# Performance work log

Hardware: AMD Instinct MI355X
Metric: run time of the kernel (lower is better)

## Reference

```python
import jax, jax.numpy as jnp
import numpy as np

D_MODEL = 256
NHEAD = 8
NUM_EXPERTS = 5
LQ, LK, BATCH = 100, 1024, 16
LN_EPS = 1e-5


def setup_inputs() -> dict:
    key = jax.random.key(0)
    ks = jax.random.split(key, 12)
    d, E = D_MODEL, NUM_EXPERTS
    s = 1.0 / np.sqrt(d)
    return {
        "tgt": jax.random.normal(ks[0], (LQ, BATCH, d), jnp.float32),
        "memory": jax.random.normal(ks[1], (LK, BATCH, d), jnp.float32),
        "query_pos": jax.random.normal(ks[2], (LQ, BATCH, d), jnp.float32),
        "pos": jax.random.normal(ks[3], (LK, BATCH, d), jnp.float32),
        # per-expert MultiheadAttention params (packed q,k,v in_proj like torch)
        "w_in": jax.random.normal(ks[4], (E, 3 * d, d), jnp.float32) * s,
        "b_in": jnp.zeros((E, 3 * d), jnp.float32),
        "w_out": jax.random.normal(ks[5], (E, d, d), jnp.float32) * s,
        "b_out": jnp.zeros((E, d), jnp.float32),
        # gating network
        "w_gate": jax.random.normal(ks[6], (E, d), jnp.float32) * s,
        "b_gate": jnp.zeros((E,), jnp.float32),
        # LayerNorm
        "ln_gamma": jnp.ones((d,), jnp.float32),
        "ln_beta": jnp.zeros((d,), jnp.float32),
    }


def _moe_cross_attn(tgt, memory, query_pos, pos, w_in, b_in, w_out, b_out,
                    w_gate, b_gate, ln_gamma, ln_beta):
    Lq, B, d = tgt.shape
    H = NHEAD
    hd = d // H
    E = w_in.shape[0]
    Lk = memory.shape[0]

    # gating over (seq*batch, d) -> softmax over experts
    gate = jax.nn.softmax(tgt @ w_gate.T + b_gate, axis=-1)  # (Lq, B, E)

    q_emb = tgt + query_pos      # (Lq, B, d)
    k_emb = memory + pos         # (Lk, B, d)

    wq, wk, wv = w_in[:, :d], w_in[:, d:2 * d], w_in[:, 2 * d:]
    bq, bk, bv = b_in[:, :d], b_in[:, d:2 * d], b_in[:, 2 * d:]

    # batched projections across all experts (replaces python loop of MHA calls)
    q = jnp.einsum('lbd,eod->elbo', q_emb, wq) + bq[:, None, None, :]
    k = jnp.einsum('sbd,eod->esbo', k_emb, wk) + bk[:, None, None, :]
    v = jnp.einsum('sbd,eod->esbo', memory, wv) + bv[:, None, None, :]

    q = q.reshape(E, Lq, B, H, hd) * (1.0 / np.sqrt(hd))
    k = k.reshape(E, Lk, B, H, hd)
    v = v.reshape(E, Lk, B, H, hd)

    scores = jnp.einsum('elbhk,esbhk->ebhls', q, k)      # (E, B, H, Lq, Lk)
    attn = jax.nn.softmax(scores, axis=-1)
    ctx = jnp.einsum('ebhls,esbhk->elbhk', attn, v).reshape(E, Lq, B, d)

    out = jnp.einsum('elbd,eod->elbo', ctx, w_out) + b_out[:, None, None, :]

    # softmax-gated weighted combine of expert outputs
    mo = jnp.einsum('lbe,elbd->lbd', gate, out)

    x = tgt + mo  # dropout is identity (p=0.0)
    mu = jnp.mean(x, axis=-1, keepdims=True)
    var = jnp.var(x, axis=-1, keepdims=True)
    return (x - mu) * jax.lax.rsqrt(var + LN_EPS) * ln_gamma + ln_beta


def reference(tgt, memory, query_pos, pos, w_in, b_in, w_out, b_out,
              w_gate, b_gate, ln_gamma, ln_beta):
    return _moe_cross_attn(tgt, memory, query_pos, pos, w_in, b_in, w_out,
                           b_out, w_gate, b_gate, ln_gamma, ln_beta)
```

## Files before the change

### kernel.cpp

```cpp
#include <hip/hip_runtime.h>


typedef __bf16 bf16x8 __attribute__((ext_vector_type(8)));
typedef float f32x4 __attribute__((ext_vector_type(4)));
typedef unsigned int u32x4 __attribute__((ext_vector_type(4)));
typedef unsigned int u32x2 __attribute__((ext_vector_type(2)));
typedef unsigned short u16x4 __attribute__((ext_vector_type(4)));
typedef unsigned short us;

__device__ __forceinline__ us f2bf(float f) {
    unsigned u = __builtin_bit_cast(unsigned, f);
    u += 0x7FFFu + ((u >> 16) & 1u);
    return (us)(u >> 16);
}

__device__ __forceinline__ unsigned pack2(float lo, float hi) {
    return (unsigned)f2bf(lo) | ((unsigned)f2bf(hi) << 16);
}

__device__ __forceinline__ float bf2f(us v) {
    unsigned u = ((unsigned)v) << 16;
    return __builtin_bit_cast(float, u);
}

__device__ __forceinline__ bf16x8 ld_bf8(const us* p) {
    return __builtin_bit_cast(bf16x8, *reinterpret_cast<const u32x4*>(p));
}

__device__ __forceinline__ void gld_lds16(const us* g, us* l) {
    __builtin_amdgcn_global_load_lds(
        (const __attribute__((address_space(1))) unsigned int*)g,
        (__attribute__((address_space(3))) unsigned int*)l, 16, 0, 0);
}

__launch_bounds__(256)
__global__ void cvt_all(const float* __restrict__ tgt, const float* __restrict__ qpos,
                        const float* __restrict__ mem, const float* __restrict__ pos,
                        const float* __restrict__ w_in, const float* __restrict__ w_out,
                        const float* __restrict__ w_gate, const float* __restrict__ b_gate,
                        us* __restrict__ Aq, us* __restrict__ Ak, us* __restrict__ Av,
                        us* __restrict__ Wb, us* __restrict__ WOb,
                        float* __restrict__ Gate)
{
    const int bid = blockIdx.x;
    const int tid = threadIdx.x;
    if (bid < 400) {
        const int i = bid * 256 + tid;
        const int lane = tid & 63;
        const int row = i >> 6;
        f32x4 a = reinterpret_cast<const f32x4*>(tgt)[i];
        f32x4 b = reinterpret_cast<const f32x4*>(qpos)[i];
        u16x4 r;
#pragma unroll
        for (int j = 0; j < 4; ++j) r[j] = f2bf(a[j] + b[j]);
        reinterpret_cast<u16x4*>(Aq)[i] = r;
        float g[5];
#pragma unroll
        for (int e = 0; e < 5; ++e) {
            f32x4 wg = *reinterpret_cast<const f32x4*>(w_gate + e * 256 + 4 * lane);
            float p = a[0] * wg[0] + a[1] * wg[1] + a[2] * wg[2] + a[3] * wg[3];
#pragma unroll
            for (int off = 32; off >= 1; off >>= 1) p += __shfl_xor(p, off, 64);
            g[e] = p + b_gate[e];
        }
        float mx = g[0];
#pragma unroll
        for (int e = 1; e < 5; ++e) mx = fmaxf(mx, g[e]);
        float sm = 0.0f;
#pragma unroll
        for (int e = 0; e < 5; ++e) { g[e] = __expf(g[e] - mx); sm += g[e]; }
        const float invs = 1.0f / sm;
        if (lane == 0) {
#pragma unroll
            for (int e = 0; e < 5; ++e) Gate[row * 5 + e] = g[e] * invs;
        }
    } else if (bid < 4496) {
        int i = (bid - 400) * 256 + tid;
        f32x4 m = reinterpret_cast<const f32x4*>(mem)[i];
        f32x4 p = reinterpret_cast<const f32x4*>(pos)[i];
        u16x4 rk, rv;
#pragma unroll
        for (int j = 0; j < 4; ++j) { rk[j] = f2bf(m[j] + p[j]); rv[j] = f2bf(m[j]); }
        reinterpret_cast<u16x4*>(Ak)[i] = rk;
        reinterpret_cast<u16x4*>(Av)[i] = rv;
    } else if (bid < 5456) {
        int i = (bid - 4496) * 256 + tid;
        f32x4 a = reinterpret_cast<const f32x4*>(w_in)[i];
        u16x4 r;
#pragma unroll
        for (int j = 0; j < 4; ++j) r[j] = f2bf(a[j]);
        const int e    = i / 49152;
        const int rem  = i % 49152;
        const int row  = rem >> 6;
        const int kq4  = rem & 63;
        const int role = row >> 8;
        const int col  = row & 255;
        const int g    = kq4 >> 1;
        const int sub  = kq4 & 1;
        const size_t dst = (size_t)(e * 3 + role) * 65536
                         + ((size_t)(g * 256 + col)) * 8 + sub * 4;
        *reinterpret_cast<u16x4*>(Wb + dst) = r;
    } else {
        int i = (bid - 5456) * 256 + tid;
        f32x4 a = reinterpret_cast<const f32x4*>(w_out)[i];
        u16x4 r;
#pragma unroll
        for (int j = 0; j < 4; ++j) r[j] = f2bf(a[j]);
        reinterpret_cast<u16x4*>(WOb)[i] = r;
    }
}

__launch_bounds__(256, 4)
__global__ void gemm_qkv(const us* __restrict__ Aq, const us* __restrict__ Ak,
                         const us* __restrict__ Av, const us* __restrict__ Wb,
                         const float* __restrict__ b_in,
                         us* __restrict__ Qb, us* __restrict__ Kb, us* __restrict__ Vb)
{
    const int rb   = blockIdx.x;
    const int col0 = blockIdx.y * 128;
    const int zr   = blockIdx.z;
    const us* A; const us* W; const float* bias; us* C;
    float scale; int M;
    if (zr < 5) {
        if (rb >= 13) return;
        A = Aq; W = Wb + (size_t)zr * 196608; bias = b_in + (size_t)zr * 768;
        C = Qb + (size_t)zr * 409600; scale = 0.17677669529663687f; M = 1600;
    } else if (zr < 10) {
        const int e = zr - 5;
        A = Ak; W = Wb + 65536 + (size_t)e * 196608; bias = b_in + (size_t)e * 768 + 256;
        C = Kb + (size_t)e * 4194304; scale = 1.0f; M = 16384;
    } else {
        const int e = zr - 10;
        A = Av; W = Wb + 131072 + (size_t)e * 196608; bias = b_in + (size_t)e * 768 + 512;
        C = Vb + (size_t)e * 4194304; scale = 1.0f; M = 16384;
    }
    const int row0 = rb * 128;

    __shared__ us As[2 * 8192];
    const int tid  = threadIdx.x;
    const int lane = tid & 63;
    const int w    = tid >> 6;
    const int l15  = lane & 15;
    const int quad = lane >> 4;
    const int wm   = (w >> 1) * 64;
    const int wn   = (w & 1) * 64;
    const int srow = lane >> 3;
    const int gofs = ((lane & 7) ^ srow) * 8;

    auto stageA = [&](int buf, int kt) {
#pragma unroll
        for (int cc = 0; cc < 4; ++cc) {
            const int c = w * 4 + cc;
            gld_lds16(A + (size_t)(row0 + c * 8 + srow) * 256 + kt * 64 + gofs,
                      &As[buf * 8192 + c * 512]);
        }
    };

    f32x4 acc[4][4] = {};

    stageA(0, 0);
    __builtin_amdgcn_sched_barrier(0);

#pragma unroll
    for (int kt = 0; kt < 4; ++kt) {
        const int cur = kt & 1;
        u32x4 bf[2][4];
#pragma unroll
        for (int kh = 0; kh < 2; ++kh)
#pragma unroll
            for (int ni = 0; ni < 4; ++ni)
                bf[kh][ni] = *reinterpret_cast<const u32x4*>(
                    W + (((size_t)(kt * 8 + kh * 4 + quad) * 256
                          + (col0 + wn + ni * 16 + l15)) * 8));
        __builtin_amdgcn_sched_barrier(0);
        if (kt < 3) stageA(cur ^ 1, kt + 1);
        __builtin_amdgcn_sched_barrier(0);
        if (kt < 3) asm volatile("s_waitcnt vmcnt(4)" ::: "memory");
        else        asm volatile("s_waitcnt vmcnt(0)" ::: "memory");
        __builtin_amdgcn_s_barrier();
        __builtin_amdgcn_sched_barrier(0);
#pragma unroll
        for (int kh = 0; kh < 2; ++kh) {
            bf16x8 af[4];
#pragma unroll
            for (int mi = 0; mi < 4; ++mi) {
                const int row = wm + mi * 16 + l15;
                const int seg = (kh * 4 + quad) ^ (row & 7);
                af[mi] = ld_bf8(&As[cur * 8192 + row * 64 + seg * 8]);
            }
#pragma unroll
            for (int mi = 0; mi < 4; ++mi)
#pragma unroll
                for (int ni = 0; ni < 4; ++ni)
                    acc[mi][ni] = __builtin_amdgcn_mfma_f32_16x16x32_bf16(
                        __builtin_bit_cast(bf16x8, bf[kh][ni]), af[mi], acc[mi][ni], 0, 0, 0);
        }
        if (kt < 3) {
            asm volatile("s_waitcnt lgkmcnt(0)" ::: "memory");
            __builtin_amdgcn_sched_barrier(0);
            __builtin_amdgcn_s_barrier();
            __builtin_amdgcn_sched_barrier(0);
        }
    }

#pragma unroll
    for (int mi = 0; mi < 4; ++mi) {
        const int row = row0 + wm + mi * 16 + l15;
        if (row < M) {
#pragma unroll
            for (int ni = 0; ni < 4; ++ni) {
                const int colb = col0 + wn + ni * 16 + quad * 4;
                const f32x4 b4 = *reinterpret_cast<const f32x4*>(bias + colb);
                u32x2 pk;
                pk[0] = pack2((acc[mi][ni][0] + b4[0]) * scale,
                              (acc[mi][ni][1] + b4[1]) * scale);
                pk[1] = pack2((acc[mi][ni][2] + b4[2]) * scale,
                              (acc[mi][ni][3] + b4[3]) * scale);
                *reinterpret_cast<u32x2*>(C + (size_t)row * 256 + colb) = pk;
            }
        }
    }
}

__launch_bounds__(256)
__global__ void gemm_og(const us* __restrict__ PO, const float* __restrict__ PL,
                        const us* __restrict__ WOb, const float* __restrict__ b_out,
                        float* __restrict__ OUTf)
{
    if (blockIdx.x >= 13) return;
    const int e = blockIdx.z;
    const us* W = WOb + (size_t)e * 65536;
    const float* bias = b_out + (size_t)e * 256;
    float* Cout = OUTf + (size_t)e * 409600;

    const int row0 = blockIdx.x * 128;
    const int col0 = blockIdx.y * 128;
    __shared__ us As[2 * 8192];
    __shared__ us Bs[2 * 8192];
    const int tid  = threadIdx.x;
    const int lane = tid & 63;
    const int w    = tid >> 6;
    const int l15  = lane & 15;
    const int quad = lane >> 4;
    const int wm   = (w >> 1) * 64;
    const int wn   = (w & 1) * 64;
    const int srow = lane >> 3;
    const int gofs = ((lane & 7) ^ srow) * 8;

    u32x4 POr[4][2];
    float Lr[4];

    auto loadA = [&](int kt) {
#pragma unroll
        for (int cc = 0; cc < 4; ++cc) {
            const int c = w * 4 + cc;
            int grow = row0 + c * 8 + srow;
            if (grow > 1599) grow = 1599;
            const int d0 = kt * 64 + gofs;
            const size_t base = (size_t)e * 409600 + (size_t)grow * 256 + d0;
#pragma unroll
            for (int s = 0; s < 2; ++s)
                POr[cc][s] = *reinterpret_cast<const u32x4*>(PO + base + (size_t)s * 2048000);
            const int l = grow >> 4, bb = grow & 15, hh = d0 >> 5;
            float L = 0.0f;
#pragma unroll
            for (int s = 0; s < 2; ++s)
                L += PL[((((size_t)s * 5 + e) * 16 + bb) * 8 + hh) * 128 + l];
            Lr[cc] = L;
        }
    };
    auto writeA = [&](int buf) {
#pragma unroll
        for (int cc = 0; cc < 4; ++cc) {
            const float inv = 1.0f / Lr[cc];
            u32x4 pk;
#pragma unroll
            for (int j = 0; j < 4; ++j) {
                float v0 = 0.0f, v1 = 0.0f;
#pragma unroll
                for (int s = 0; s < 2; ++s) {
                    const unsigned u = POr[cc][s][j];
                    v0 += __builtin_bit_cast(float, u << 16);
                    v1 += __builtin_bit_cast(float, u & 0xffff0000u);
                }
                pk[j] = pack2(v0 * inv, v1 * inv);
            }
            *reinterpret_cast<u32x4*>(&As[buf * 8192 + (w * 4 + cc) * 512 + lane * 8]) = pk;
        }
    };
    auto loadW = [&](int buf, int kt) {
#pragma unroll
        for (int cc = 0; cc < 4; ++cc) {
            const int c = w * 4 + cc;
            const int row = c * 8 + srow;
            gld_lds16(W + (size_t)(col0 + row) * 256 + kt * 64 + gofs,
                      &Bs[buf * 8192 + c * 512]);
        }
    };

    loadA(0);
    loadW(0, 0);
    writeA(0);
    __syncthreads();

    f32x4 acc[4][4] = {};

#pragma unroll
    for (int kt = 0; kt < 4; ++kt) {
        const int cur = kt & 1;
        if (kt < 3) {
            loadA(kt + 1);
            loadW(cur ^ 1, kt + 1);
        }
#pragma unroll
        for (int kh = 0; kh < 2; ++kh) {
            bf16x8 af[4], bf[4];
#pragma unroll
            for (int mi = 0; mi < 4; ++mi) {
                const int row = wm + mi * 16 + l15;
                const int seg = (kh * 4 + quad) ^ (row & 7);
                af[mi] = ld_bf8(&As[cur * 8192 + row * 64 + seg * 8]);
            }
#pragma unroll
            for (int ni = 0; ni < 4; ++ni) {
                const int col = wn + ni * 16 + l15;
                const int seg = (kh * 4 + quad) ^ (col & 7);
                bf[ni] = ld_bf8(&Bs[cur * 8192 + col * 64 + seg * 8]);
            }
#pragma unroll
            for (int mi = 0; mi < 4; ++mi)
#pragma unroll
                for (int ni = 0; ni < 4; ++ni)
                    acc[mi][ni] = __builtin_amdgcn_mfma_f32_16x16x32_bf16(bf[ni], af[mi], acc[mi][ni], 0, 0, 0);
        }
        if (kt < 3) {
            writeA(cur ^ 1);
            __syncthreads();
        }
    }

#pragma unroll
    for (int mi = 0; mi < 4; ++mi) {
        const int row = row0 + wm + mi * 16 + l15;
        if (row < 1600) {
#pragma unroll
            for (int ni = 0; ni < 4; ++ni) {
                const int colb = col0 + wn + ni * 16 + quad * 4;
                const f32x4 b4 = *reinterpret_cast<const f32x4*>(bias + colb);
                f32x4 v;
#pragma unroll
                for (int r = 0; r < 4; ++r) v[r] = acc[mi][ni][r] + b4[r];
                *reinterpret_cast<f32x4*>(Cout + (size_t)row * 256 + colb) = v;
            }
        }
    }
}

__device__ __forceinline__ int vrow(int d) { return d * 264 + 8 * (d >> 3); }

__launch_bounds__(512)
__global__ void attn(const us* __restrict__ Qb, const us* __restrict__ Kb,
                     const us* __restrict__ Vb, us* __restrict__ PO,
                     float* __restrict__ PL)
{
    const int z = blockIdx.x;
    const int h = blockIdx.y;
    const int sp = blockIdx.z;
    const int e = z >> 4, b = z & 15;
    const int tid  = threadIdx.x;
    const int w    = tid >> 6;
    const int lane = tid & 63;
    const int l15  = lane & 15, quad = lane >> 4;
    __shared__ us Ks[256 * 32];
    __shared__ us Vs[8464];
    __shared__ us Ps[7][2][16 * 40];

    u32x4 qraw = {0u, 0u, 0u, 0u};
    if (w < 7) {
        const int l = w * 16 + l15;
        if (l < 100)
            qraw = *reinterpret_cast<const u32x4*>(
                Qb + ((size_t)((e * 100 + l) * 16 + b)) * 256 + h * 32 + quad * 8);
    }
    const bf16x8 qf = __builtin_bit_cast(bf16x8, qraw);

    const f32x4 zacc = {};
    f32x4 o0 = {}, o1 = {};
    float lsum = 0.0f;

    for (int sc = 0; sc < 2; ++sc) {
        const int key0 = (sp * 2 + sc) * 256;
        if (sc) __syncthreads();
        {
            const int kl  = lane >> 2;
            const int seg = lane & 3;
            const us* kg = Kb + ((size_t)((e * 1024 + key0 + w * 16 + kl) * 16 + b)) * 256
                              + h * 32 + seg * 8;
            gld_lds16(kg, &Ks[w * 512]);
            gld_lds16(kg + (size_t)128 * 16 * 256, &Ks[4096 + w * 512]);

            const int kv = tid >> 2;
            const int sg = tid & 3;
            const us* vg = Vb + ((size_t)((e * 1024 + key0 + kv) * 16 + b)) * 256
                              + h * 32 + sg * 8;
            u32x4 v0 = *reinterpret_cast<const u32x4*>(vg);
            u32x4 v1 = *reinterpret_cast<const u32x4*>(vg + (size_t)128 * 16 * 256);
#pragma unroll
            for (int j = 0; j < 4; ++j) {
                const int d0 = sg * 8 + 2 * j;
                const int e0 = vrow(d0);
                const int e1 = e0 + 264;
                Vs[e0 + kv]       = (us)(v0[j] & 0xffff);
                Vs[e1 + kv]       = (us)(v0[j] >> 16);
                Vs[e0 + 128 + kv] = (us)(v1[j] & 0xffff);
                Vs[e1 + 128 + kv] = (us)(v1[j] >> 16);
            }
        }
        __syncthreads();

        if (w < 7) {
            auto qk = [&](int c) {
                bf16x8 kf0 = ld_bf8(&Ks[(c * 32 + l15) * 32 + quad * 8]);
                bf16x8 kf1 = ld_bf8(&Ks[(c * 32 + 16 + l15) * 32 + quad * 8]);
                f32x4 s0 = __builtin_amdgcn_mfma_f32_16x16x32_bf16(kf0, qf, zacc, 0, 0, 0);
                f32x4 s1 = __builtin_amdgcn_mfma_f32_16x16x32_bf16(kf1, qf, zacc, 0, 0, 0);
                float p0[4], p1[4];
#pragma unroll
                for (int r = 0; r < 4; ++r) {
                    p0[r] = __expf(s0[r]);
                    p1[r] = __expf(s1[r]);
                    lsum += p0[r] + p1[r];
                }
                u32x2 w0, w1;
                w0[0] = pack2(p0[0], p0[1]);
                w0[1] = pack2(p0[2], p0[3]);
                w1[0] = pack2(p1[0], p1[1]);
                w1[1] = pack2(p1[2], p1[3]);
                us* psb = &Ps[w][c & 1][0];
                *reinterpret_cast<u32x2*>(&psb[l15 * 40 + quad * 4])      = w0;
                *reinterpret_cast<u32x2*>(&psb[l15 * 40 + 16 + quad * 4]) = w1;
            };
            auto pv = [&](int c) {
                bf16x8 pf  = ld_bf8(&Ps[w][c & 1][l15 * 40 + quad * 8]);
                bf16x8 vf0 = ld_bf8(&Vs[vrow(l15) + c * 32 + quad * 8]);
                bf16x8 vf1 = ld_bf8(&Vs[vrow(16 + l15) + c * 32 + quad * 8]);
                o0 = __builtin_amdgcn_mfma_f32_16x16x32_bf16(pf, vf0, o0, 0, 0, 0);
                o1 = __builtin_amdgcn_mfma_f32_16x16x32_bf16(pf, vf1, o1, 0, 0, 0);
            };
            qk(0);
#pragma unroll
            for (int c = 1; c < 8; ++c) {
                qk(c);
                pv(c - 1);
            }
            pv(7);
        }
    }

    if (w >= 7) return;

    lsum += __shfl_xor(lsum, 16, 64);
    lsum += __shfl_xor(lsum, 32, 64);

#pragma unroll
    for (int r = 0; r < 4; ++r) {
        const int row = w * 16 + quad * 4 + r;
        if (row < 100) {
            const size_t o = (((size_t)((sp * 5 + e) * 100 + row)) * 16 + b) * 256 + h * 32;
            PO[o + l15]      = f2bf(o0[r]);
            PO[o + 16 + l15] = f2bf(o1[r]);
        }
    }
    const int q = w * 16 + l15;
    if (quad == 0 && q < 100)
        PL[((((size_t)sp * 5 + e) * 16 + b) * 8 + h) * 128 + q] = lsum;
}

__launch_bounds__(256)
__global__ void finalize(const float* __restrict__ tgt, const float* __restrict__ Gate,
                         const float* __restrict__ OUTf,
                         const float* __restrict__ gamma, const float* __restrict__ beta,
                         float* __restrict__ out)
{
    const int row = blockIdx.x;
    const int d = threadIdx.x;
    __shared__ float red[8];
    const float t = tgt[(size_t)row * 256 + d];

    float mo = 0.0f;
#pragma unroll
    for (int e = 0; e < 5; ++e)
        mo += Gate[row * 5 + e] * OUTf[((size_t)e * 1600 + row) * 256 + d];
    const float x = t + mo;

    float p1 = x, p2 = x * x;
#pragma unroll
    for (int off = 32; off >= 1; off >>= 1) {
        p1 += __shfl_xor(p1, off, 64);
        p2 += __shfl_xor(p2, off, 64);
    }
    if ((d & 63) == 0) { red[d >> 6] = p1; red[4 + (d >> 6)] = p2; }
    __syncthreads();
    const float mean = (red[0] + red[1] + red[2] + red[3]) * (1.0f / 256.0f);
    const float msq  = (red[4] + red[5] + red[6] + red[7]) * (1.0f / 256.0f);
    const float var  = msq - mean * mean;

    out[(size_t)row * 256 + d] = (x - mean) * rsqrtf(var + 1e-5f) * gamma[d] + beta[d];
}

extern "C" void kernel_launch(void* const* d_in, const int* in_sizes, int n_in,
                              void* d_out, int out_size, void* d_ws, size_t ws_size,
                              hipStream_t stream)
{
    const float* tgt    = (const float*)d_in[0];
    const float* mem    = (const float*)d_in[1];
    const float* qpos   = (const float*)d_in[2];
    const float* pos    = (const float*)d_in[3];
    const float* w_in   = (const float*)d_in[4];
    const float* b_in   = (const float*)d_in[5];
    const float* w_out  = (const float*)d_in[6];
    const float* b_out  = (const float*)d_in[7];
    const float* w_gate = (const float*)d_in[8];
    const float* b_gate = (const float*)d_in[9];
    const float* ln_g   = (const float*)d_in[10];
    const float* ln_b   = (const float*)d_in[11];
    float* out = (float*)d_out;

    char* p = (char*)d_ws;
    auto alloc = [&](size_t n) { char* r = p; p += (n + 255) & ~(size_t)255; return r; };

    us* Aq   = (us*)alloc(409600ull * 2);
    us* Ak   = (us*)alloc(4194304ull * 2);
    us* Av   = (us*)alloc(4194304ull * 2);
    us* Wb   = (us*)alloc(983040ull * 2);
    us* WOb  = (us*)alloc(327680ull * 2);
    us* Qb   = (us*)alloc(5ull * 409600 * 2);
    us* Kb   = (us*)alloc(5ull * 4194304 * 2);
    us* Vb   = (us*)alloc(5ull * 4194304 * 2);
    float* OUTf  = (float*)alloc(5ull * 409600 * 4);
    float* Gate  = (float*)alloc(1600ull * 5 * 4);
    us*    PO = (us*)d_ws;
    float* PL = (float*)((char*)d_ws + 8192000);

    cvt_all<<<5776, 256, 0, stream>>>(tgt, qpos, mem, pos, w_in, w_out,
                                      w_gate, b_gate, Aq, Ak, Av, Wb, WOb, Gate);

    gemm_qkv<<<dim3(128, 2, 15), 256, 0, stream>>>(Aq, Ak, Av, Wb, b_in, Qb, Kb, Vb);

    attn<<<dim3(80, 8, 2), 512, 0, stream>>>(Qb, Kb, Vb, PO, PL);

    gemm_og<<<dim3(16, 2, 5), 256, 0, stream>>>(PO, PL, WOb, b_out, OUTf);

    finalize<<<1600, 256, 0, stream>>>(tgt, Gate, OUTf, ln_g, ln_b, out);
}
```

Before: 192.4 us.

## Store K/V projections in head-major layout for contiguous attention loads

The projection GEMM epilogue for K and V experts (zr>=5) now writes output in an [e][h][b][key][32] layout instead of row-major [key][b][256]. The attention kernel reads K and V tiles from this layout, so each (e,b,h) block streams contiguous 64-byte rows instead of strided 64-byte pieces spaced 8KB apart. This is meant to improve DRAM/cache locality of the attention loads, at the cost of scattered 8-byte stores in the GEMM epilogue. The new addressing assumes M is an exact multiple of the tile, since the row<M bounds check was dropped for that branch.

```diff
diff --git a/kernel.cpp b/kernel.cpp
--- a/kernel.cpp
+++ b/kernel.cpp
@@ -203,10 +203,30 @@
         }
     }
 
-#pragma unroll
-    for (int mi = 0; mi < 4; ++mi) {
-        const int row = row0 + wm + mi * 16 + l15;
-        if (row < M) {
+    if (zr < 5) {
+#pragma unroll
+        for (int mi = 0; mi < 4; ++mi) {
+            const int row = row0 + wm + mi * 16 + l15;
+            if (row < M) {
+#pragma unroll
+                for (int ni = 0; ni < 4; ++ni) {
+                    const int colb = col0 + wn + ni * 16 + quad * 4;
+                    const f32x4 b4 = *reinterpret_cast<const f32x4*>(bias + colb);
+                    u32x2 pk;
+                    pk[0] = pack2((acc[mi][ni][0] + b4[0]) * scale,
+                                  (acc[mi][ni][1] + b4[1]) * scale);
+                    pk[1] = pack2((acc[mi][ni][2] + b4[2]) * scale,
+                                  (acc[mi][ni][3] + b4[3]) * scale);
+                    *reinterpret_cast<u32x2*>(C + (size_t)row * 256 + colb) = pk;
+                }
+            }
+        }
+    } else {
+#pragma unroll
+        for (int mi = 0; mi < 4; ++mi) {
+            const int row = row0 + wm + mi * 16 + l15;
+            const int key = row >> 4;
+            const int b   = row & 15;
 #pragma unroll
             for (int ni = 0; ni < 4; ++ni) {
                 const int colb = col0 + wn + ni * 16 + quad * 4;
@@ -216,7 +236,9 @@
                               (acc[mi][ni][1] + b4[1]) * scale);
                 pk[1] = pack2((acc[mi][ni][2] + b4[2]) * scale,
                               (acc[mi][ni][3] + b4[3]) * scale);
-                *reinterpret_cast<u32x2*>(C + (size_t)row * 256 + colb) = pk;
+                const size_t dst = ((((size_t)(colb >> 5) * 16 + b) * 1024) + key) * 32
+                                 + (colb & 31);
+                *reinterpret_cast<u32x2*>(C + dst) = pk;
             }
         }
     }
@@ -375,6 +397,8 @@
     __shared__ us Vs[8464];
     __shared__ us Ps[7][2][16 * 40];
 
+    const size_t hvbase = (((size_t)(e * 8 + h) * 16 + b) * 1024) * 32;
+
     u32x4 qraw = {0u, 0u, 0u, 0u};
     if (w < 7) {
         const int l = w * 16 + l15;
@@ -394,17 +418,15 @@
         {
             const int kl  = lane >> 2;
             const int seg = lane & 3;
-            const us* kg = Kb + ((size_t)((e * 1024 + key0 + w * 16 + kl) * 16 + b)) * 256
-                              + h * 32 + seg * 8;
+            const us* kg = Kb + hvbase + (size_t)(key0 + w * 16 + kl) * 32 + seg * 8;
             gld_lds16(kg, &Ks[w * 512]);
-            gld_lds16(kg + (size_t)128 * 16 * 256, &Ks[4096 + w * 512]);
+            gld_lds16(kg + (size_t)128 * 32, &Ks[4096 + w * 512]);
 
             const int kv = tid >> 2;
             const int sg = tid & 3;
-            const us* vg = Vb + ((size_t)((e * 1024 + key0 + kv) * 16 + b)) * 256
-                              + h * 32 + sg * 8;
+            const us* vg = Vb + hvbase + (size_t)(key0 + kv) * 32 + sg * 8;
             u32x4 v0 = *reinterpret_cast<const u32x4*>(vg);
-            u32x4 v1 = *reinterpret_cast<const u32x4*>(vg + (size_t)128 * 16 * 256);
+            u32x4 v1 = *reinterpret_cast<const u32x4*>(vg + (size_t)128 * 32);
 #pragma unroll
             for (int j = 0; j < 4; ++j) {
                 const int d0 = sg * 8 + 2 * j;
```

Result: no change. 194.8 us (+1.2%).

## Widen QKV GEMM tiles to full 256 columns and drop attention key split

Applied to the files above, without the earlier changes.

The QKV projection now uses 512-thread blocks that each compute all 256 output columns for a 128-row tile. This halves the A-tile reloads and the grid size. The attention kernel no longer splits the 1024 keys across two blocks. Each block loops over all four 256-key chunks, which removes the partial-sum write and the reduction in the output-projection GEMM. In exchange, attention parallelism falls to 640 blocks and the GEMM blocks carry higher register and LDS pressure, which could hurt occupancy.

```diff
diff --git a/kernel.cpp b/kernel.cpp
--- a/kernel.cpp
+++ b/kernel.cpp
@@ -110,15 +110,14 @@
     }
 }
 
-__launch_bounds__(256, 4)
+__launch_bounds__(512, 4)
 __global__ void gemm_qkv(const us* __restrict__ Aq, const us* __restrict__ Ak,
                          const us* __restrict__ Av, const us* __restrict__ Wb,
                          const float* __restrict__ b_in,
                          us* __restrict__ Qb, us* __restrict__ Kb, us* __restrict__ Vb)
 {
-    const int rb   = blockIdx.x;
-    const int col0 = blockIdx.y * 128;
-    const int zr   = blockIdx.z;
+    const int rb = blockIdx.x;
+    const int zr = blockIdx.y;
     const us* A; const us* W; const float* bias; us* C;
     float scale; int M;
     if (zr < 5) {
@@ -142,15 +141,15 @@
     const int w    = tid >> 6;
     const int l15  = lane & 15;
     const int quad = lane >> 4;
-    const int wm   = (w >> 1) * 64;
-    const int wn   = (w & 1) * 64;
+    const int wm   = (w >> 2) * 64;
+    const int wn   = (w & 3) * 64;
     const int srow = lane >> 3;
     const int gofs = ((lane & 7) ^ srow) * 8;
 
     auto stageA = [&](int buf, int kt) {
 #pragma unroll
-        for (int cc = 0; cc < 4; ++cc) {
-            const int c = w * 4 + cc;
+        for (int cc = 0; cc < 2; ++cc) {
+            const int c = w * 2 + cc;
             gld_lds16(A + (size_t)(row0 + c * 8 + srow) * 256 + kt * 64 + gofs,
                       &As[buf * 8192 + c * 512]);
         }
@@ -171,11 +170,11 @@
             for (int ni = 0; ni < 4; ++ni)
                 bf[kh][ni] = *reinterpret_cast<const u32x4*>(
                     W + (((size_t)(kt * 8 + kh * 4 + quad) * 256
-                          + (col0 + wn + ni * 16 + l15)) * 8));
+                          + (wn + ni * 16 + l15)) * 8));
         __builtin_amdgcn_sched_barrier(0);
         if (kt < 3) stageA(cur ^ 1, kt + 1);
         __builtin_amdgcn_sched_barrier(0);
-        if (kt < 3) asm volatile("s_waitcnt vmcnt(4)" ::: "memory");
+        if (kt < 3) asm volatile("s_waitcnt vmcnt(2)" ::: "memory");
         else        asm volatile("s_waitcnt vmcnt(0)" ::: "memory");
         __builtin_amdgcn_s_barrier();
         __builtin_amdgcn_sched_barrier(0);
@@ -209,7 +208,7 @@
         if (row < M) {
 #pragma unroll
             for (int ni = 0; ni < 4; ++ni) {
-                const int colb = col0 + wn + ni * 16 + quad * 4;
+                const int colb = wn + ni * 16 + quad * 4;
                 const f32x4 b4 = *reinterpret_cast<const f32x4*>(bias + colb);
                 u32x2 pk;
                 pk[0] = pack2((acc[mi][ni][0] + b4[0]) * scale,
@@ -247,7 +246,7 @@
     const int srow = lane >> 3;
     const int gofs = ((lane & 7) ^ srow) * 8;
 
-    u32x4 POr[4][2];
+    u32x4 POr[4];
     float Lr[4];
 
     auto loadA = [&](int kt) {
@@ -257,16 +256,10 @@
             int grow = row0 + c * 8 + srow;
             if (grow > 1599) grow = 1599;
             const int d0 = kt * 64 + gofs;
-            const size_t base = (size_t)e * 409600 + (size_t)grow * 256 + d0;
-#pragma unroll
-            for (int s = 0; s < 2; ++s)
-                POr[cc][s] = *reinterpret_cast<const u32x4*>(PO + base + (size_t)s * 2048000);
+            POr[cc] = *reinterpret_cast<const u32x4*>(
+                PO + (size_t)e * 409600 + (size_t)grow * 256 + d0);
             const int l = grow >> 4, bb = grow & 15, hh = d0 >> 5;
-            float L = 0.0f;
-#pragma unroll
-            for (int s = 0; s < 2; ++s)
-                L += PL[((((size_t)s * 5 + e) * 16 + bb) * 8 + hh) * 128 + l];
-            Lr[cc] = L;
+            Lr[cc] = PL[(((size_t)e * 16 + bb) * 8 + hh) * 128 + l];
         }
     };
     auto writeA = [&](int buf) {
@@ -276,13 +269,9 @@
             u32x4 pk;
 #pragma unroll
             for (int j = 0; j < 4; ++j) {
-                float v0 = 0.0f, v1 = 0.0f;
-#pragma unroll
-                for (int s = 0; s < 2; ++s) {
-                    const unsigned u = POr[cc][s][j];
-                    v0 += __builtin_bit_cast(float, u << 16);
-                    v1 += __builtin_bit_cast(float, u & 0xffff0000u);
-                }
+                const unsigned u = POr[cc][j];
+                const float v0 = __builtin_bit_cast(float, u << 16);
+                const float v1 = __builtin_bit_cast(float, u & 0xffff0000u);
                 pk[j] = pack2(v0 * inv, v1 * inv);
             }
             *reinterpret_cast<u32x4*>(&As[buf * 8192 + (w * 4 + cc) * 512 + lane * 8]) = pk;
@@ -365,7 +354,6 @@
 {
     const int z = blockIdx.x;
     const int h = blockIdx.y;
-    const int sp = blockIdx.z;
     const int e = z >> 4, b = z & 15;
     const int tid  = threadIdx.x;
     const int w    = tid >> 6;
@@ -388,8 +376,8 @@
     f32x4 o0 = {}, o1 = {};
     float lsum = 0.0f;
 
-    for (int sc = 0; sc < 2; ++sc) {
-        const int key0 = (sp * 2 + sc) * 256;
+    for (int sc = 0; sc < 4; ++sc) {
+        const int key0 = sc * 256;
         if (sc) __syncthreads();
         {
             const int kl  = lane >> 2;
@@ -466,14 +454,14 @@
     for (int r = 0; r < 4; ++r) {
         const int row = w * 16 + quad * 4 + r;
         if (row < 100) {
-            const size_t o = (((size_t)((sp * 5 + e) * 100 + row)) * 16 + b) * 256 + h * 32;
+            const size_t o = (((size_t)(e * 100 + row)) * 16 + b) * 256 + h * 32;
             PO[o + l15]      = f2bf(o0[r]);
             PO[o + 16 + l15] = f2bf(o1[r]);
         }
     }
     const int q = w * 16 + l15;
     if (quad == 0 && q < 100)
-        PL[((((size_t)sp * 5 + e) * 16 + b) * 8 + h) * 128 + q] = lsum;
+        PL[(((size_t)e * 16 + b) * 8 + h) * 128 + q] = lsum;
 }
 
 __launch_bounds__(256)
@@ -540,14 +528,14 @@
     float* OUTf  = (float*)alloc(5ull * 409600 * 4);
     float* Gate  = (float*)alloc(1600ull * 5 * 4);
     us*    PO = (us*)d_ws;
-    float* PL = (float*)((char*)d_ws + 8192000);
+    float* PL = (float*)((char*)d_ws + 4096000);
 
     cvt_all<<<5776, 256, 0, stream>>>(tgt, qpos, mem, pos, w_in, w_out,
                                       w_gate, b_gate, Aq, Ak, Av, Wb, WOb, Gate);
 
-    gemm_qkv<<<dim3(128, 2, 15), 256, 0, stream>>>(Aq, Ak, Av, Wb, b_in, Qb, Kb, Vb);
-
-    attn<<<dim3(80, 8, 2), 512, 0, stream>>>(Qb, Kb, Vb, PO, PL);
+    gemm_qkv<<<dim3(128, 15), 512, 0, stream>>>(Aq, Ak, Av, Wb, b_in, Qb, Kb, Vb);
+
+    attn<<<dim3(80, 8), 512, 0, stream>>>(Qb, Kb, Vb, PO, PL);
 
     gemm_og<<<dim3(16, 2, 5), 256, 0, stream>>>(PO, PL, WOb, b_out, OUTf);
 
```

Result: slower. 199.1 us (+3.5%).

## Fuse K/V projection into attention kernel, drop materialized K/V buffers

Applied to the files above, without the earlier changes.

Removes the K and V projection GEMM and their large bf16 intermediate buffers. Each attention block now computes its own 256-key by 32-dim K and V head slices with MFMA directly from the converted memory/pos activations and the packed weights, then writes them into shared memory. This avoids writing and re-reading roughly 80 MB of K/V through HBM. The cost is redundant work: the same key rows are re-read for every head, and the projection loads go straight from global memory with no LDS staging. Only the Q projection remains a separate GEMM, and the PO/PL workspace now gets its own allocations.

```diff
diff --git a/kernel.cpp b/kernel.cpp
--- a/kernel.cpp
+++ b/kernel.cpp
@@ -111,29 +111,18 @@
 }
 
 __launch_bounds__(256, 4)
-__global__ void gemm_qkv(const us* __restrict__ Aq, const us* __restrict__ Ak,
-                         const us* __restrict__ Av, const us* __restrict__ Wb,
-                         const float* __restrict__ b_in,
-                         us* __restrict__ Qb, us* __restrict__ Kb, us* __restrict__ Vb)
+__global__ void gemm_q(const us* __restrict__ Aq, const us* __restrict__ Wb,
+                       const float* __restrict__ b_in, us* __restrict__ Qb)
 {
     const int rb   = blockIdx.x;
     const int col0 = blockIdx.y * 128;
-    const int zr   = blockIdx.z;
-    const us* A; const us* W; const float* bias; us* C;
-    float scale; int M;
-    if (zr < 5) {
-        if (rb >= 13) return;
-        A = Aq; W = Wb + (size_t)zr * 196608; bias = b_in + (size_t)zr * 768;
-        C = Qb + (size_t)zr * 409600; scale = 0.17677669529663687f; M = 1600;
-    } else if (zr < 10) {
-        const int e = zr - 5;
-        A = Ak; W = Wb + 65536 + (size_t)e * 196608; bias = b_in + (size_t)e * 768 + 256;
-        C = Kb + (size_t)e * 4194304; scale = 1.0f; M = 16384;
-    } else {
-        const int e = zr - 10;
-        A = Av; W = Wb + 131072 + (size_t)e * 196608; bias = b_in + (size_t)e * 768 + 512;
-        C = Vb + (size_t)e * 4194304; scale = 1.0f; M = 16384;
-    }
+    const int e    = blockIdx.z;
+    const us* A = Aq;
+    const us* W = Wb + (size_t)e * 196608;
+    const float* bias = b_in + (size_t)e * 768;
+    us* C = Qb + (size_t)e * 409600;
+    const float scale = 0.17677669529663687f;
+    const int M = 1600;
     const int row0 = rb * 128;
 
     __shared__ us As[2 * 8192];
@@ -359,9 +348,10 @@
 __device__ __forceinline__ int vrow(int d) { return d * 264 + 8 * (d >> 3); }
 
 __launch_bounds__(512)
-__global__ void attn(const us* __restrict__ Qb, const us* __restrict__ Kb,
-                     const us* __restrict__ Vb, us* __restrict__ PO,
-                     float* __restrict__ PL)
+__global__ void attn(const us* __restrict__ Qb, const us* __restrict__ Ak,
+                     const us* __restrict__ Av, const us* __restrict__ Wb,
+                     const float* __restrict__ b_in,
+                     us* __restrict__ PO, float* __restrict__ PL)
 {
     const int z = blockIdx.x;
     const int h = blockIdx.y;
@@ -375,6 +365,11 @@
     __shared__ us Vs[8464];
     __shared__ us Ps[7][2][16 * 40];
 
+    const us* Wk = Wb + (size_t)(e * 3 + 1) * 65536;
+    const us* Wv = Wb + (size_t)(e * 3 + 2) * 65536;
+    const float* bk_base = b_in + e * 768 + 256 + h * 32;
+    const float* bv_base = b_in + e * 768 + 512 + h * 32;
+
     u32x4 qraw = {0u, 0u, 0u, 0u};
     if (w < 7) {
         const int l = w * 16 + l15;
@@ -388,73 +383,106 @@
     f32x4 o0 = {}, o1 = {};
     float lsum = 0.0f;
 
+    auto compute = [&]() {
+        auto qk = [&](int c) {
+            bf16x8 kf0 = ld_bf8(&Ks[(c * 32 + l15) * 32 + quad * 8]);
+            bf16x8 kf1 = ld_bf8(&Ks[(c * 32 + 16 + l15) * 32 + quad * 8]);
+            f32x4 s0 = __builtin_amdgcn_mfma_f32_16x16x32_bf16(kf0, qf, zacc, 0, 0, 0);
+            f32x4 s1 = __builtin_amdgcn_mfma_f32_16x16x32_bf16(kf1, qf, zacc, 0, 0, 0);
+            float p0[4], p1[4];
+#pragma unroll
+            for (int r = 0; r < 4; ++r) {
+                p0[r] = __expf(s0[r]);
+                p1[r] = __expf(s1[r]);
+                lsum += p0[r] + p1[r];
+            }
+            u32x2 w0, w1;
+            w0[0] = pack2(p0[0], p0[1]);
+            w0[1] = pack2(p0[2], p0[3]);
+            w1[0] = pack2(p1[0], p1[1]);
+            w1[1] = pack2(p1[2], p1[3]);
+            us* psb = &Ps[w][c & 1][0];
+            *reinterpret_cast<u32x2*>(&psb[l15 * 40 + quad * 4])      = w0;
+            *reinterpret_cast<u32x2*>(&psb[l15 * 40 + 16 + quad * 4]) = w1;
+        };
+        auto pv = [&](int c) {
+            bf16x8 pf  = ld_bf8(&Ps[w][c & 1][l15 * 40 + quad * 8]);
+            bf16x8 vf0 = ld_bf8(&Vs[vrow(l15) + c * 32 + quad * 8]);
+            bf16x8 vf1 = ld_bf8(&Vs[vrow(16 + l15) + c * 32 + quad * 8]);
+            o0 = __builtin_amdgcn_mfma_f32_16x16x32_bf16(pf, vf0, o0, 0, 0, 0);
+            o1 = __builtin_amdgcn_mfma_f32_16x16x32_bf16(pf, vf1, o1, 0, 0, 0);
+        };
+        qk(0);
+#pragma unroll
+        for (int c = 1; c < 8; ++c) {
+            qk(c);
+            pv(c - 1);
+        }
+        pv(7);
+    };
+
     for (int sc = 0; sc < 2; ++sc) {
         const int key0 = (sp * 2 + sc) * 256;
         if (sc) __syncthreads();
+
         {
-            const int kl  = lane >> 2;
-            const int seg = lane & 3;
-            const us* kg = Kb + ((size_t)((e * 1024 + key0 + w * 16 + kl) * 16 + b)) * 256
-                              + h * 32 + seg * 8;
-            gld_lds16(kg, &Ks[w * 512]);
-            gld_lds16(kg + (size_t)128 * 16 * 256, &Ks[4096 + w * 512]);
-
-            const int kv = tid >> 2;
-            const int sg = tid & 3;
-            const us* vg = Vb + ((size_t)((e * 1024 + key0 + kv) * 16 + b)) * 256
-                              + h * 32 + sg * 8;
-            u32x4 v0 = *reinterpret_cast<const u32x4*>(vg);
-            u32x4 v1 = *reinterpret_cast<const u32x4*>(vg + (size_t)128 * 16 * 256);
-#pragma unroll
-            for (int j = 0; j < 4; ++j) {
-                const int d0 = sg * 8 + 2 * j;
-                const int e0 = vrow(d0);
-                const int e1 = e0 + 264;
-                Vs[e0 + kv]       = (us)(v0[j] & 0xffff);
-                Vs[e1 + kv]       = (us)(v0[j] >> 16);
-                Vs[e0 + 128 + kv] = (us)(v1[j] & 0xffff);
-                Vs[e1 + 128 + kv] = (us)(v1[j] >> 16);
+            const int wkey = w * 32;
+            f32x4 ka[2][2] = {};
+            f32x4 va[2][2] = {};
+#pragma unroll
+            for (int kt = 0; kt < 4; ++kt)
+#pragma unroll
+                for (int kh = 0; kh < 2; ++kh) {
+                    const int g = kt * 8 + kh * 4 + quad;
+                    u32x4 afk[2], afv[2], bk[2], bv[2];
+#pragma unroll
+                    for (int mi = 0; mi < 2; ++mi) {
+                        const size_t arow =
+                            (size_t)((key0 + wkey + mi * 16 + l15) * 16 + b) * 256
+                            + kt * 64 + kh * 32 + quad * 8;
+                        afk[mi] = *reinterpret_cast<const u32x4*>(Ak + arow);
+                        afv[mi] = *reinterpret_cast<const u32x4*>(Av + arow);
+                    }
+#pragma unroll
+                    for (int ni = 0; ni < 2; ++ni) {
+                        const size_t wof =
+                            ((size_t)g * 256 + (h * 32 + ni * 16 + l15)) * 8;
+                        bk[ni] = *reinterpret_cast<const u32x4*>(Wk + wof);
+                        bv[ni] = *reinterpret_cast<const u32x4*>(Wv + wof);
+                    }
+#pragma unroll
+                    for (int mi = 0; mi < 2; ++mi)
+#pragma unroll
+                        for (int ni = 0; ni < 2; ++ni) {
+                            ka[mi][ni] = __builtin_amdgcn_mfma_f32_16x16x32_bf16(
+                                __builtin_bit_cast(bf16x8, bk[ni]),
+                                __builtin_bit_cast(bf16x8, afk[mi]), ka[mi][ni], 0, 0, 0);
+                            va[mi][ni] = __builtin_amdgcn_mfma_f32_16x16x32_bf16(
+                                __builtin_bit_cast(bf16x8, bv[ni]),
+                                __builtin_bit_cast(bf16x8, afv[mi]), va[mi][ni], 0, 0, 0);
+                        }
+                }
+#pragma unroll
+            for (int mi = 0; mi < 2; ++mi) {
+                const int key = wkey + mi * 16 + l15;
+#pragma unroll
+                for (int ni = 0; ni < 2; ++ni) {
+                    const int d = ni * 16 + quad * 4;
+                    const f32x4 bk4 = *reinterpret_cast<const f32x4*>(bk_base + d);
+                    const f32x4 bv4 = *reinterpret_cast<const f32x4*>(bv_base + d);
+                    u32x2 pk;
+                    pk[0] = pack2(ka[mi][ni][0] + bk4[0], ka[mi][ni][1] + bk4[1]);
+                    pk[1] = pack2(ka[mi][ni][2] + bk4[2], ka[mi][ni][3] + bk4[3]);
+                    *reinterpret_cast<u32x2*>(&Ks[key * 32 + d]) = pk;
+#pragma unroll
+                    for (int r = 0; r < 4; ++r)
+                        Vs[vrow(d + r) + key] = f2bf(va[mi][ni][r] + bv4[r]);
+                }
             }
         }
         __syncthreads();
 
-        if (w < 7) {
-            auto qk = [&](int c) {
-                bf16x8 kf0 = ld_bf8(&Ks[(c * 32 + l15) * 32 + quad * 8]);
-                bf16x8 kf1 = ld_bf8(&Ks[(c * 32 + 16 + l15) * 32 + quad * 8]);
-                f32x4 s0 = __builtin_amdgcn_mfma_f32_16x16x32_bf16(kf0, qf, zacc, 0, 0, 0);
-                f32x4 s1 = __builtin_amdgcn_mfma_f32_16x16x32_bf16(kf1, qf, zacc, 0, 0, 0);
-                float p0[4], p1[4];
-#pragma unroll
-                for (int r = 0; r < 4; ++r) {
-                    p0[r] = __expf(s0[r]);
-                    p1[r] = __expf(s1[r]);
-                    lsum += p0[r] + p1[r];
-                }
-                u32x2 w0, w1;
-                w0[0] = pack2(p0[0], p0[1]);
-                w0[1] = pack2(p0[2], p0[3]);
-                w1[0] = pack2(p1[0], p1[1]);
-                w1[1] = pack2(p1[2], p1[3]);
-                us* psb = &Ps[w][c & 1][0];
-                *reinterpret_cast<u32x2*>(&psb[l15 * 40 + quad * 4])      = w0;
-                *reinterpret_cast<u32x2*>(&psb[l15 * 40 + 16 + quad * 4]) = w1;
-            };
-            auto pv = [&](int c) {
-                bf16x8 pf  = ld_bf8(&Ps[w][c & 1][l15 * 40 + quad * 8]);
-                bf16x8 vf0 = ld_bf8(&Vs[vrow(l15) + c * 32 + quad * 8]);
-                bf16x8 vf1 = ld_bf8(&Vs[vrow(16 + l15) + c * 32 + quad * 8]);
-                o0 = __builtin_amdgcn_mfma_f32_16x16x32_bf16(pf, vf0, o0, 0, 0, 0);
-                o1 = __builtin_amdgcn_mfma_f32_16x16x32_bf16(pf, vf1, o1, 0, 0, 0);
-            };
-            qk(0);
-#pragma unroll
-            for (int c = 1; c < 8; ++c) {
-                qk(c);
-                pv(c - 1);
-            }
-            pv(7);
-        }
+        if (w < 7) compute();
     }
 
     if (w >= 7) return;
@@ -535,19 +563,17 @@
     us* Wb   = (us*)alloc(983040ull * 2);
     us* WOb  = (us*)alloc(327680ull * 2);
     us* Qb   = (us*)alloc(5ull * 409600 * 2);
-    us* Kb   = (us*)alloc(5ull * 4194304 * 2);
-    us* Vb   = (us*)alloc(5ull * 4194304 * 2);
-    float* OUTf  = (float*)alloc(5ull * 409600 * 4);
-    float* Gate  = (float*)alloc(1600ull * 5 * 4);
-    us*    PO = (us*)d_ws;
-    float* PL = (float*)((char*)d_ws + 8192000);
+    float* OUTf = (float*)alloc(5ull * 409600 * 4);
+    float* Gate = (float*)alloc(1600ull * 5 * 4);
+    us*    PO = (us*)alloc(4096000ull * 2);
+    float* PL = (float*)alloc(163840ull * 4);
 
     cvt_all<<<5776, 256, 0, stream>>>(tgt, qpos, mem, pos, w_in, w_out,
                                       w_gate, b_gate, Aq, Ak, Av, Wb, WOb, Gate);
 
-    gemm_qkv<<<dim3(128, 2, 15), 256, 0, stream>>>(Aq, Ak, Av, Wb, b_in, Qb, Kb, Vb);
-
-    attn<<<dim3(80, 8, 2), 512, 0, stream>>>(Qb, Kb, Vb, PO, PL);
+    gemm_q<<<dim3(13, 2, 5), 256, 0, stream>>>(Aq, Wb, b_in, Qb);
+
+    attn<<<dim3(80, 8, 2), 512, 0, stream>>>(Qb, Ak, Av, Wb, b_in, PO, PL);
 
     gemm_og<<<dim3(16, 2, 5), 256, 0, stream>>>(PO, PL, WOb, b_out, OUTf);
 
```

Result: slower. 242.9 us (+26.2%).
